# Kernel tuning notes

Measured on AMD Instinct MI355X. Metric: run time of the kernel, lower is better.

Reference implementation:

```python
import jax, jax.numpy as jnp
import numpy as np

IN_FEATURES = 4096
OUT_FEATURES = 16384


def setup_inputs() -> dict:
    key = jax.random.key(0)
    k_x, k_w = jax.random.split(key)
    x = jax.random.normal(k_x, (8192, IN_FEATURES), dtype=jnp.float32)
    weight = jax.random.normal(k_w, (OUT_FEATURES, IN_FEATURES), dtype=jnp.float32)
    return {"x": x, "weight": weight}


def ternary_quantize(weight):
    # scale = mean(|W|) clamped; quantize to {-1,0,1}*scale
    scale = jnp.maximum(jnp.mean(jnp.abs(weight)), 1e-8)
    q = jnp.round(jnp.clip(weight / scale, -1.0, 1.0)) * scale
    return q


def reference(x, weight):
    qw = ternary_quantize(weight)  # [out, in]
    # F.linear: x @ W^T
    return jnp.einsum('ti,oi->to', x, qw)
```

## Files before the change

### kernel.cpp

```cpp
#include <hip/hip_runtime.h>
#include <hip/hip_bf16.h>
#include <stdint.h>

typedef __attribute__((ext_vector_type(4))) int i32x4;

#define M_DIM 8192
#define K_DIM 4096
#define N_DIM 16384
#define NELEM_W ((long)N_DIM * (long)K_DIM)
#define NELEM_X ((long)M_DIM * (long)K_DIM)


__device__ __forceinline__ void g2l16(const void* g, void* l) {
  __builtin_amdgcn_global_load_lds(
      (const __attribute__((address_space(1))) unsigned int*)g,
      (__attribute__((address_space(3))) unsigned int*)l, 16, 0, 0);
}


__global__ void reduce_absw(const float4* __restrict__ w4, double* __restrict__ partials, int n4) {
  const int tid = threadIdx.x;
  double s = 0.0;
  const int stride = gridDim.x * blockDim.x;
  for (int i = blockIdx.x * blockDim.x + tid; i < n4; i += stride) {
    float4 v = w4[i];
    s += (double)fabsf(v.x);
    s += (double)fabsf(v.y);
    s += (double)fabsf(v.z);
    s += (double)fabsf(v.w);
  }
  __shared__ double sd[256];
  sd[tid] = s;
  __syncthreads();
  for (int off = 128; off > 0; off >>= 1) {
    if (tid < off) sd[tid] += sd[tid + off];
    __syncthreads();
  }
  if (tid == 0) partials[blockIdx.x] = sd[0];
}

__global__ void finalize_scale(const double* __restrict__ partials, float* __restrict__ sp) {
  const int tid = threadIdx.x;
  double s = 0.0;
#pragma unroll
  for (int j = 0; j < 8; ++j) s += partials[tid * 8 + j];
  __shared__ double sd[256];
  sd[tid] = s;
  __syncthreads();
  for (int off = 128; off > 0; off >>= 1) {
    if (tid < off) sd[tid] += sd[tid + off];
    __syncthreads();
  }
  if (tid == 0) {
    double mean = sd[0] / (double)NELEM_W;
    float sc = (float)mean;
    if (sc < 1e-8f) sc = 1e-8f;
    sp[0] = sc;
  }
}


__global__ void quant_w_i8(const float4* __restrict__ w4, char* __restrict__ q,
                           const float* __restrict__ sp, int n4) {
  const float sc = sp[0];
  const int stride = gridDim.x * blockDim.x;
  for (int i = blockIdx.x * blockDim.x + threadIdx.x; i < n4; i += stride) {
    float4 v = w4[i];
    char4 o;
    o.x = (char)rintf(fminf(fmaxf(v.x / sc, -1.f), 1.f));
    o.y = (char)rintf(fminf(fmaxf(v.y / sc, -1.f), 1.f));
    o.z = (char)rintf(fminf(fmaxf(v.z / sc, -1.f), 1.f));
    o.w = (char)rintf(fminf(fmaxf(v.w / sc, -1.f), 1.f));
    *(char4*)(q + (long)i * 4) = o;
  }
}


__global__ __launch_bounds__(256)
void quant_x_i8(const float* __restrict__ x, char* __restrict__ xq,
                float* __restrict__ s_row) {
  const int row = blockIdx.x;
  const int tid = threadIdx.x;
  const float4* xr = (const float4*)(x + (long)row * K_DIM);
  float4 v[4];
  float m = 0.f;
#pragma unroll
  for (int k = 0; k < 4; ++k) {
    v[k] = xr[tid + 256 * k];
    m = fmaxf(m, fmaxf(fmaxf(fabsf(v[k].x), fabsf(v[k].y)),
                       fmaxf(fabsf(v[k].z), fabsf(v[k].w))));
  }
  __shared__ float red[256];
  red[tid] = m;
  __syncthreads();
  for (int off = 128; off > 0; off >>= 1) {
    if (tid < off) red[tid] = fmaxf(red[tid], red[tid + off]);
    __syncthreads();
  }
  const float mx = red[0];
  const float inv = (mx > 0.f) ? (127.f / mx) : 0.f;
  if (tid == 0) s_row[row] = (mx > 0.f) ? (mx / 127.f) : 0.f;
  char4* out = (char4*)(xq + (long)row * K_DIM);
#pragma unroll
  for (int k = 0; k < 4; ++k) {
    char4 o;
    o.x = (char)fminf(fmaxf(rintf(v[k].x * inv), -127.f), 127.f);
    o.y = (char)fminf(fmaxf(rintf(v[k].y * inv), -127.f), 127.f);
    o.z = (char)fminf(fmaxf(rintf(v[k].z * inv), -127.f), 127.f);
    o.w = (char)fminf(fmaxf(rintf(v[k].w * inv), -127.f), 127.f);
    out[tid + 256 * k] = o;
  }
}


template<int MH, int NH>
__device__ __forceinline__ void mfmaq(i32x4 (&acc)[8][4], const i32x4 (&a)[8], const i32x4 (&bfr)[8]) {
#pragma unroll
  for (int im = 0; im < 4; ++im) {
#pragma unroll
    for (int in = 0; in < 2; ++in) {
      const int m = MH * 4 + im, n = NH * 2 + in;
      acc[m][n] = __builtin_amdgcn_mfma_i32_16x16x64_i8(a[im * 2 + 0], bfr[n * 2 + 0], acc[m][n], 0, 0, 0);
      acc[m][n] = __builtin_amdgcn_mfma_i32_16x16x64_i8(a[im * 2 + 1], bfr[n * 2 + 1], acc[m][n], 0, 0, 0);
    }
  }
}

#define FENCE asm volatile("" ::: "memory")
#define BAR do { FENCE; __builtin_amdgcn_s_barrier(); FENCE; } while (0)
#define VMW6 asm volatile("s_waitcnt vmcnt(6)" ::: "memory")
#define VMW0 asm volatile("s_waitcnt vmcnt(0)" ::: "memory")
#define PRIO1 __builtin_amdgcn_s_setprio(1)
#define PRIO0 __builtin_amdgcn_s_setprio(0)

#define STG_A(bb, h, kt) do { \
    const char* g_ = Ac + aG + (unsigned)(h) * 524288u + (unsigned)(kt) * 128u; \
    char* l_ = lds + (unsigned)(bb) * 32768u + (unsigned)(h) * 16384u + ldsT; \
    g2l16(g_, l_); g2l16(g_ + 262144u, l_ + 8192u); \
  } while (0)
#define STG_B(bb, h, kt) do { \
    const char* g_ = Bc + bG + (unsigned)(h) * 524288u + (unsigned)(kt) * 128u; \
    char* l_ = lds + 65536u + (unsigned)(bb) * 32768u + (unsigned)(h) * 16384u + ldsT; \
    g2l16(g_, l_); g2l16(g_ + 262144u, l_ + 8192u); \
  } while (0)

#define LDA_(d, bb, m, ks) d = *(const i32x4*)(lds + Abase##bb + (unsigned)(m) * 2048u + frk + coff##ks)
#define LDB_(d, bb, n, ks) d = *(const i32x4*)(lds + Bbase##bb + (unsigned)(n) * 2048u + frk + coff##ks)

#define RD_A03(bb) do { \
    LDA_(a[0], bb, 0, 0); LDA_(a[1], bb, 0, 1); LDA_(a[2], bb, 1, 0); LDA_(a[3], bb, 1, 1); \
    LDA_(a[4], bb, 2, 0); LDA_(a[5], bb, 2, 1); LDA_(a[6], bb, 3, 0); LDA_(a[7], bb, 3, 1); \
  } while (0)
#define RD_A47(bb) do { \
    LDA_(a[0], bb, 4, 0); LDA_(a[1], bb, 4, 1); LDA_(a[2], bb, 5, 0); LDA_(a[3], bb, 5, 1); \
    LDA_(a[4], bb, 6, 0); LDA_(a[5], bb, 6, 1); LDA_(a[6], bb, 7, 0); LDA_(a[7], bb, 7, 1); \
  } while (0)
#define RD_BALL(bb) do { \
    LDB_(bfr[0], bb, 0, 0); LDB_(bfr[1], bb, 0, 1); LDB_(bfr[2], bb, 1, 0); LDB_(bfr[3], bb, 1, 1); \
    LDB_(bfr[4], bb, 2, 0); LDB_(bfr[5], bb, 2, 1); LDB_(bfr[6], bb, 3, 0); LDB_(bfr[7], bb, 3, 1); \
  } while (0)

#define MFMA_PHASE(MH, NH) do { BAR; PRIO1; mfmaq<MH, NH>(acc, a, bfr); PRIO0; BAR; } while (0)

__global__ __launch_bounds__(512, 2)
void gemm_i8(const char* __restrict__ A, const char* __restrict__ B,
             float* __restrict__ C, const float* __restrict__ sp,
             const float* __restrict__ s_row) {
  extern __shared__ char lds[];

  const int tid = threadIdx.x;
  const int wave = tid >> 6, lane = tid & 63;
  const int fr = lane & 15, fq = lane >> 4;
  const int wr = wave >> 2;
  const int wc = wave & 3;

  int wgid = blockIdx.x;
  wgid = (wgid & 7) * ((int)gridDim.x >> 3) + (wgid >> 3);
  const int bm = wgid >> 6;
  const int bn = wgid & 63;

  const int r0 = tid >> 3;
  const int pslot = tid & 7;
  const int lslot = pslot ^ (r0 & 7);
  const unsigned aG = (unsigned)(bm * 256 + r0) * (unsigned)K_DIM + (unsigned)lslot * 16u;
  const unsigned bG = (unsigned)(bn * 256 + r0) * (unsigned)K_DIM + (unsigned)lslot * 16u;
  const unsigned ldsT = (unsigned)tid * 16u;
  const char* Ac = A;
  const char* Bc = B;

  const unsigned axor = (unsigned)(fr & 7) << 4;
  const unsigned coff0 = ((unsigned)(fq * 16)) ^ axor;
  const unsigned coff1 = ((unsigned)(64 + fq * 16)) ^ axor;
  const unsigned frk = (unsigned)fr * 128u;
  const unsigned Abase0 = (unsigned)(wr * 16384);
  const unsigned Abase1 = (unsigned)(32768 + wr * 16384);
  const unsigned Bhalf = (unsigned)(65536 + (wc >> 1) * 16384 + (wc & 1) * 8192);
  const unsigned Bbase0 = Bhalf;
  const unsigned Bbase1 = Bhalf + 32768u;

  i32x4 acc[8][4] = {};
  i32x4 a[8], bfr[8];

  STG_A(0, 0, 0); STG_A(0, 1, 0);
  STG_B(0, 0, 0); STG_B(0, 1, 0);
  STG_B(1, 0, 1); STG_B(1, 1, 1); STG_A(1, 0, 1);
  VMW6;
  BAR;

#pragma unroll 1
  for (int i = 0; i < 15; ++i) {
    const int t1 = 2 * i + 1, t2 = 2 * i + 2, t3 = 2 * i + 3;

    RD_A03(0); RD_BALL(0);
    STG_A(1, 1, t1);
    MFMA_PHASE(0, 0);
    STG_B(0, 0, t2);
    MFMA_PHASE(0, 1);
    RD_A47(0);
    STG_B(0, 1, t2);
    MFMA_PHASE(1, 1);
    STG_A(0, 0, t2);
    VMW6;
    MFMA_PHASE(1, 0);
    RD_A03(1); RD_BALL(1);
    STG_A(0, 1, t2);
    MFMA_PHASE(0, 0);
    STG_B(1, 0, t3);
    MFMA_PHASE(0, 1);
    RD_A47(1);
    STG_B(1, 1, t3);
    MFMA_PHASE(1, 1);
    STG_A(1, 0, t3);
    VMW6;
    MFMA_PHASE(1, 0);
  }

  {
    RD_A03(0); RD_BALL(0);
    STG_A(1, 1, 31);
    MFMA_PHASE(0, 0);
    MFMA_PHASE(0, 1);
    RD_A47(0);
    MFMA_PHASE(1, 1);
    VMW0;
    MFMA_PHASE(1, 0);
    RD_A03(1); RD_BALL(1);
    MFMA_PHASE(0, 0);
    MFMA_PHASE(0, 1);
    RD_A47(1);
    MFMA_PHASE(1, 1);
    MFMA_PHASE(1, 0);
  }

  const float sw = sp[0];
  const int crow0 = bm * 256 + wr * 128 + fq * 4;
  const int ccol0 = bn * 256 + wc * 64 + fr;
#pragma unroll
  for (int m = 0; m < 8; ++m) {
#pragma unroll
    for (int j = 0; j < 4; ++j) {
      const int row = crow0 + m * 16 + j;
      const float sc = s_row[row] * sw;
#pragma unroll
      for (int n = 0; n < 4; ++n) {
        C[(long)row * N_DIM + (ccol0 + n * 16)] = (float)acc[m][n][j] * sc;
      }
    }
  }
}


typedef __hip_bfloat16 bf16;
typedef __attribute__((ext_vector_type(8))) short short8;
typedef __attribute__((ext_vector_type(4))) float f32x4;

__device__ __forceinline__ unsigned short f2bf(float f) {
  unsigned int u = __float_as_uint(f);
  u += 0x7FFFu + ((u >> 16) & 1u);
  return (unsigned short)(u >> 16);
}

__global__ __launch_bounds__(256)
void gemm_fly(const float* __restrict__ X, const float* __restrict__ W,
              float* __restrict__ C, const float* __restrict__ sp) {
  __shared__ alignas(16) bf16 As[128 * 32];
  __shared__ alignas(16) bf16 Bs[128 * 32];

  const int tid = threadIdx.x;
  const int wave = tid >> 6;
  const int lane = tid & 63;

  int wgid = blockIdx.x;
  wgid = (wgid & 7) * ((int)gridDim.x >> 3) + (wgid >> 3);
  const int nbn = N_DIM / 128;
  const int bm = wgid / nbn;
  const int bn = wgid % nbn;

  const float sc = sp[0];

  const int wr = (wave >> 1) * 64;
  const int wc = (wave & 1) * 64;
  const int fr = lane & 15;
  const int fq = lane >> 4;
  const char* AsB = (const char*)As;
  const char* BsB = (const char*)Bs;
  const unsigned aoff = (unsigned)((wr + fr) * 64 + fq * 16);
  const unsigned boff = (unsigned)((wc + fr) * 64 + fq * 16);

  f32x4 acc[4][4] = {};

  for (int kt = 0; kt < K_DIM; kt += 32) {
#pragma unroll
    for (int r = 0; r < 4; ++r) {
      int e = r * 1024 + tid * 4;
      int row = e >> 5;
      int k4 = e & 31;
      float4 xv = *(const float4*)(X + (long)(bm * 128 + row) * K_DIM + kt + k4);
      ushort4 xb;
      xb.x = f2bf(xv.x); xb.y = f2bf(xv.y); xb.z = f2bf(xv.z); xb.w = f2bf(xv.w);
      *(ushort4*)(As + e) = xb;
      float4 wv = *(const float4*)(W + (long)(bn * 128 + row) * K_DIM + kt + k4);
      ushort4 wb;
      wb.x = f2bf(rintf(fminf(fmaxf(wv.x / sc, -1.f), 1.f)));
      wb.y = f2bf(rintf(fminf(fmaxf(wv.y / sc, -1.f), 1.f)));
      wb.z = f2bf(rintf(fminf(fmaxf(wv.z / sc, -1.f), 1.f)));
      wb.w = f2bf(rintf(fminf(fmaxf(wv.w / sc, -1.f), 1.f)));
      *(ushort4*)(Bs + e) = wb;
    }
    __syncthreads();

    short8 a[4], b[4];
#pragma unroll
    for (int m = 0; m < 4; ++m)
      a[m] = *(const short8*)(AsB + aoff + m * (16 * 64));
#pragma unroll
    for (int n = 0; n < 4; ++n)
      b[n] = *(const short8*)(BsB + boff + n * (16 * 64));
#pragma unroll
    for (int m = 0; m < 4; ++m)
#pragma unroll
      for (int n = 0; n < 4; ++n)
        acc[m][n] = __builtin_amdgcn_mfma_f32_16x16x32_bf16(a[m], b[n], acc[m][n], 0, 0, 0);

    __syncthreads();
  }

  const long crow0 = (long)(bm * 128 + wr + fq * 4);
  const int ccol0 = bn * 128 + wc + fr;
#pragma unroll
  for (int m = 0; m < 4; ++m)
#pragma unroll
    for (int n = 0; n < 4; ++n)
#pragma unroll
      for (int j = 0; j < 4; ++j) {
        long row = crow0 + (long)(m * 16 + j);
        int col = ccol0 + n * 16;
        C[row * N_DIM + col] = acc[m][n][j] * sc;
      }
}


extern "C" void kernel_launch(void* const* d_in, const int* in_sizes, int n_in,
                              void* d_out, int out_size, void* d_ws, size_t ws_size,
                              hipStream_t stream) {
  const float* x = (const float*)d_in[0];
  const float* w = (const float*)d_in[1];
  float* out = (float*)d_out;

  char* ws = (char*)d_ws;
  double* partials = (double*)ws;
  float* sp = (float*)(ws + 16384);
  const size_t SROW_OFF = 32768;
  const size_t WQ_OFF = SROW_OFF + 32768;
  const size_t XQ_OFF = WQ_OFF + (size_t)NELEM_W;
  const size_t NEEDED = XQ_OFF + (size_t)NELEM_X;

  reduce_absw<<<2048, 256, 0, stream>>>((const float4*)w, partials, (int)(NELEM_W / 4));
  finalize_scale<<<1, 256, 0, stream>>>(partials, sp);

  if (ws_size >= NEEDED) {
    float* s_row = (float*)(ws + SROW_OFF);
    char* wq = ws + WQ_OFF;
    char* xq = ws + XQ_OFF;
    quant_w_i8<<<2048, 256, 0, stream>>>((const float4*)w, wq, sp, (int)(NELEM_W / 4));
    quant_x_i8<<<M_DIM, 256, 0, stream>>>(x, xq, s_row);

    static const int lds_bytes = 131072;
    (void)hipFuncSetAttribute((const void*)gemm_i8,
                              hipFuncAttributeMaxDynamicSharedMemorySize, lds_bytes);
    const int grid = (M_DIM / 256) * (N_DIM / 256);
    gemm_i8<<<grid, 512, lds_bytes, stream>>>(xq, wq, out, sp, s_row);
  } else {
    const int grid = (M_DIM / 128) * (N_DIM / 128);
    gemm_fly<<<grid, 256, 0, stream>>>(x, w, out, sp);
  }
}
```

Baseline: 681.1 us.

## Switch int8 GEMM to 32x32x32 MFMA with reworked LDS reads and barriers

Replaces the 16x16x64 int8 MFMA tiles with 32x32x32 int8 MFMA, cutting the number of MFMA instructions and LDS fragment loads per wave. Fragment reads are regrouped into two phases per buffer with explicit lgkmcnt waits, and each MFMA group now has a single barrier instead of two. The epilogue is rewritten for the 32x32 accumulator layout. Fewer barriers and reads should reduce stalls, but this risks LDS bank conflicts with the new lane mapping and ordering hazards from the looser synchronisation.

```diff
diff --git a/kernel.cpp b/kernel.cpp
--- a/kernel.cpp
+++ b/kernel.cpp
@@ -3,6 +3,7 @@
 #include <stdint.h>
 
 typedef __attribute__((ext_vector_type(4))) int i32x4;
+typedef __attribute__((ext_vector_type(16))) int i32x16;
 
 #define M_DIM 8192
 #define K_DIM 4096
@@ -113,23 +114,11 @@
 }
 
 
-template<int MH, int NH>
-__device__ __forceinline__ void mfmaq(i32x4 (&acc)[8][4], const i32x4 (&a)[8], const i32x4 (&bfr)[8]) {
-#pragma unroll
-  for (int im = 0; im < 4; ++im) {
-#pragma unroll
-    for (int in = 0; in < 2; ++in) {
-      const int m = MH * 4 + im, n = NH * 2 + in;
-      acc[m][n] = __builtin_amdgcn_mfma_i32_16x16x64_i8(a[im * 2 + 0], bfr[n * 2 + 0], acc[m][n], 0, 0, 0);
-      acc[m][n] = __builtin_amdgcn_mfma_i32_16x16x64_i8(a[im * 2 + 1], bfr[n * 2 + 1], acc[m][n], 0, 0, 0);
-    }
-  }
-}
-
 #define FENCE asm volatile("" ::: "memory")
 #define BAR do { FENCE; __builtin_amdgcn_s_barrier(); FENCE; } while (0)
 #define VMW6 asm volatile("s_waitcnt vmcnt(6)" ::: "memory")
 #define VMW0 asm volatile("s_waitcnt vmcnt(0)" ::: "memory")
+#define LGKM0 asm volatile("s_waitcnt lgkmcnt(0)" ::: "memory")
 #define PRIO1 __builtin_amdgcn_s_setprio(1)
 #define PRIO0 __builtin_amdgcn_s_setprio(0)
 
@@ -144,23 +133,33 @@
     g2l16(g_, l_); g2l16(g_ + 262144u, l_ + 8192u); \
   } while (0)
 
-#define LDA_(d, bb, m, ks) d = *(const i32x4*)(lds + Abase##bb + (unsigned)(m) * 2048u + frk + coff##ks)
-#define LDB_(d, bb, n, ks) d = *(const i32x4*)(lds + Bbase##bb + (unsigned)(n) * 2048u + frk + coff##ks)
-
-#define RD_A03(bb) do { \
-    LDA_(a[0], bb, 0, 0); LDA_(a[1], bb, 0, 1); LDA_(a[2], bb, 1, 0); LDA_(a[3], bb, 1, 1); \
-    LDA_(a[4], bb, 2, 0); LDA_(a[5], bb, 2, 1); LDA_(a[6], bb, 3, 0); LDA_(a[7], bb, 3, 1); \
-  } while (0)
-#define RD_A47(bb) do { \
-    LDA_(a[0], bb, 4, 0); LDA_(a[1], bb, 4, 1); LDA_(a[2], bb, 5, 0); LDA_(a[3], bb, 5, 1); \
-    LDA_(a[4], bb, 6, 0); LDA_(a[5], bb, 6, 1); LDA_(a[6], bb, 7, 0); LDA_(a[7], bb, 7, 1); \
-  } while (0)
-#define RD_BALL(bb) do { \
-    LDB_(bfr[0], bb, 0, 0); LDB_(bfr[1], bb, 0, 1); LDB_(bfr[2], bb, 1, 0); LDB_(bfr[3], bb, 1, 1); \
-    LDB_(bfr[4], bb, 2, 0); LDB_(bfr[5], bb, 2, 1); LDB_(bfr[6], bb, 3, 0); LDB_(bfr[7], bb, 3, 1); \
-  } while (0)
-
-#define MFMA_PHASE(MH, NH) do { BAR; PRIO1; mfmaq<MH, NH>(acc, a, bfr); PRIO0; BAR; } while (0)
+#define RD_P1(Ar, Br) do { \
+    b[0] = *(const i32x4*)(lds + (Br) + cof0);          a[0] = *(const i32x4*)(lds + (Ar) + cof0); \
+    a[4] = *(const i32x4*)(lds + (Ar) + 4096u + cof0); \
+    b[1] = *(const i32x4*)(lds + (Br) + cof1);          a[1] = *(const i32x4*)(lds + (Ar) + cof1); \
+    a[5] = *(const i32x4*)(lds + (Ar) + 4096u + cof1); \
+    b[2] = *(const i32x4*)(lds + (Br) + cof2);          a[2] = *(const i32x4*)(lds + (Ar) + cof2); \
+    a[6] = *(const i32x4*)(lds + (Ar) + 4096u + cof2); \
+    b[3] = *(const i32x4*)(lds + (Br) + cof3);          a[3] = *(const i32x4*)(lds + (Ar) + cof3); \
+    a[7] = *(const i32x4*)(lds + (Ar) + 4096u + cof3); \
+    b[4] = *(const i32x4*)(lds + (Br) + 4096u + cof0);  b[5] = *(const i32x4*)(lds + (Br) + 4096u + cof1); \
+    b[6] = *(const i32x4*)(lds + (Br) + 4096u + cof2);  b[7] = *(const i32x4*)(lds + (Br) + 4096u + cof3); \
+  } while (0)
+
+#define RD_P3(Ar) do { \
+    a[0] = *(const i32x4*)(lds + (Ar) + 8192u + cof0);  a[4] = *(const i32x4*)(lds + (Ar) + 12288u + cof0); \
+    a[1] = *(const i32x4*)(lds + (Ar) + 8192u + cof1);  a[5] = *(const i32x4*)(lds + (Ar) + 12288u + cof1); \
+    a[2] = *(const i32x4*)(lds + (Ar) + 8192u + cof2);  a[6] = *(const i32x4*)(lds + (Ar) + 12288u + cof2); \
+    a[3] = *(const i32x4*)(lds + (Ar) + 8192u + cof3);  a[7] = *(const i32x4*)(lds + (Ar) + 12288u + cof3); \
+  } while (0)
+
+#define MF8(NH, accA, accB) do { \
+    _Pragma("unroll") \
+    for (int ks = 0; ks < 4; ++ks) { \
+      accA = __builtin_amdgcn_mfma_i32_32x32x32_i8(a[ks],     b[(NH) * 4 + ks], accA, 0, 0, 0); \
+      accB = __builtin_amdgcn_mfma_i32_32x32x32_i8(a[4 + ks], b[(NH) * 4 + ks], accB, 0, 0, 0); \
+    } \
+  } while (0)
 
 __global__ __launch_bounds__(512, 2)
 void gemm_i8(const char* __restrict__ A, const char* __restrict__ B,
@@ -170,7 +169,8 @@
 
   const int tid = threadIdx.x;
   const int wave = tid >> 6, lane = tid & 63;
-  const int fr = lane & 15, fq = lane >> 4;
+  const int rl = lane & 31;
+  const int kh = lane >> 5;
   const int wr = wave >> 2;
   const int wc = wave & 3;
 
@@ -188,18 +188,21 @@
   const char* Ac = A;
   const char* Bc = B;
 
-  const unsigned axor = (unsigned)(fr & 7) << 4;
-  const unsigned coff0 = ((unsigned)(fq * 16)) ^ axor;
-  const unsigned coff1 = ((unsigned)(64 + fq * 16)) ^ axor;
-  const unsigned frk = (unsigned)fr * 128u;
-  const unsigned Abase0 = (unsigned)(wr * 16384);
-  const unsigned Abase1 = (unsigned)(32768 + wr * 16384);
-  const unsigned Bhalf = (unsigned)(65536 + (wc >> 1) * 16384 + (wc & 1) * 8192);
-  const unsigned Bbase0 = Bhalf;
-  const unsigned Bbase1 = Bhalf + 32768u;
-
-  i32x4 acc[8][4] = {};
-  i32x4 a[8], bfr[8];
+  const unsigned x7 = (unsigned)(lane & 7);
+  const unsigned cof0 = ((0u | (unsigned)kh) ^ x7) << 4;
+  const unsigned cof1 = ((2u | (unsigned)kh) ^ x7) << 4;
+  const unsigned cof2 = ((4u | (unsigned)kh) ^ x7) << 4;
+  const unsigned cof3 = ((6u | (unsigned)kh) ^ x7) << 4;
+  const unsigned frk = (unsigned)rl * 128u;
+  const unsigned A0r = (unsigned)(wr * 16384) + frk;
+  const unsigned A1r = 32768u + (unsigned)(wr * 16384) + frk;
+  const unsigned bofs = (unsigned)((wc >> 1) * 16384 + (wc & 1) * 8192);
+  const unsigned B0r = 65536u + bofs + frk;
+  const unsigned B1r = 98304u + bofs + frk;
+
+  i32x16 c00 = {}, c01 = {}, c10 = {}, c11 = {};
+  i32x16 c20 = {}, c21 = {}, c30 = {}, c31 = {};
+  i32x4 a[8], b[8];
 
   STG_A(0, 0, 0); STG_A(0, 1, 0);
   STG_B(0, 0, 0); STG_B(0, 1, 0);
@@ -211,62 +214,80 @@
   for (int i = 0; i < 15; ++i) {
     const int t1 = 2 * i + 1, t2 = 2 * i + 2, t3 = 2 * i + 3;
 
-    RD_A03(0); RD_BALL(0);
     STG_A(1, 1, t1);
-    MFMA_PHASE(0, 0);
+    RD_P1(A0r, B0r);
+    PRIO1; MF8(0, c00, c10); PRIO0;
+    LGKM0;
+    BAR;
     STG_B(0, 0, t2);
-    MFMA_PHASE(0, 1);
-    RD_A47(0);
+    PRIO1; MF8(1, c01, c11); PRIO0;
+    BAR;
     STG_B(0, 1, t2);
-    MFMA_PHASE(1, 1);
+    RD_P3(A0r);
+    PRIO1; MF8(1, c21, c31); PRIO0;
+    BAR;
     STG_A(0, 0, t2);
+    PRIO1; MF8(0, c20, c30); PRIO0;
     VMW6;
-    MFMA_PHASE(1, 0);
-    RD_A03(1); RD_BALL(1);
+    BAR;
     STG_A(0, 1, t2);
-    MFMA_PHASE(0, 0);
+    RD_P1(A1r, B1r);
+    PRIO1; MF8(0, c00, c10); PRIO0;
+    LGKM0;
+    BAR;
     STG_B(1, 0, t3);
-    MFMA_PHASE(0, 1);
-    RD_A47(1);
+    PRIO1; MF8(1, c01, c11); PRIO0;
+    BAR;
     STG_B(1, 1, t3);
-    MFMA_PHASE(1, 1);
+    RD_P3(A1r);
+    PRIO1; MF8(1, c21, c31); PRIO0;
+    BAR;
     STG_A(1, 0, t3);
+    PRIO1; MF8(0, c20, c30); PRIO0;
     VMW6;
-    MFMA_PHASE(1, 0);
+    BAR;
   }
 
   {
-    RD_A03(0); RD_BALL(0);
     STG_A(1, 1, 31);
-    MFMA_PHASE(0, 0);
-    MFMA_PHASE(0, 1);
-    RD_A47(0);
-    MFMA_PHASE(1, 1);
+    RD_P1(A0r, B0r);
+    PRIO1; MF8(0, c00, c10); PRIO0;
+    LGKM0;
+    BAR;
+    PRIO1; MF8(1, c01, c11); PRIO0;
+    BAR;
+    RD_P3(A0r);
+    PRIO1; MF8(1, c21, c31); PRIO0;
+    BAR;
+    PRIO1; MF8(0, c20, c30); PRIO0;
     VMW0;
-    MFMA_PHASE(1, 0);
-    RD_A03(1); RD_BALL(1);
-    MFMA_PHASE(0, 0);
-    MFMA_PHASE(0, 1);
-    RD_A47(1);
-    MFMA_PHASE(1, 1);
-    MFMA_PHASE(1, 0);
+    BAR;
+    RD_P1(A1r, B1r);
+    PRIO1; MF8(0, c00, c10); PRIO0;
+    PRIO1; MF8(1, c01, c11); PRIO0;
+    RD_P3(A1r);
+    PRIO1; MF8(1, c21, c31); PRIO0;
+    PRIO1; MF8(0, c20, c30); PRIO0;
   }
 
   const float sw = sp[0];
-  const int crow0 = bm * 256 + wr * 128 + fq * 4;
-  const int ccol0 = bn * 256 + wc * 64 + fr;
-#pragma unroll
-  for (int m = 0; m < 8; ++m) {
-#pragma unroll
-    for (int j = 0; j < 4; ++j) {
-      const int row = crow0 + m * 16 + j;
-      const float sc = s_row[row] * sw;
-#pragma unroll
-      for (int n = 0; n < 4; ++n) {
-        C[(long)row * N_DIM + (ccol0 + n * 16)] = (float)acc[m][n][j] * sc;
-      }
-    }
-  }
+  const int crow0 = bm * 256 + wr * 128;
+  const int ccol0 = bn * 256 + wc * 64;
+#define EPI2(ccA, ccB, mt) do { \
+    _Pragma("unroll") \
+    for (int r = 0; r < 16; ++r) { \
+      const int grow = crow0 + (mt) * 32 + (r & 3) + 8 * (r >> 2) + 4 * kh; \
+      const float scl = s_row[grow] * sw; \
+      float* rowp = C + (long)grow * N_DIM + ccol0 + rl; \
+      rowp[0]  = (float)ccA[r] * scl; \
+      rowp[32] = (float)ccB[r] * scl; \
+    } \
+  } while (0)
+  EPI2(c00, c01, 0);
+  EPI2(c10, c11, 1);
+  EPI2(c20, c21, 2);
+  EPI2(c30, c31, 3);
+#undef EPI2
 }
 
 
```

Measured after the change: 1.785 ms. 2.62x slower.

## Halve barriers per MFMA phase and interleave LDS reads with MFMA issue

Applied to the files above, without the earlier changes.

Replaces the two-barriers-per-phase MFMA_PHASE macro with a schedule of one barrier per phase. Global-to-LDS stages and LDS fragment reads now issue before or between MFMA groups, with explicit lgkmcnt(0) waits only where a buffer is about to be overwritten. The aim is to cut barrier stalls and let LDS traffic overlap the matrix-core work. The risk is a race if the reordered barriers no longer protect the double-buffered LDS tiles, and the compiler may still insert its own waits.

```diff
diff --git a/kernel.cpp b/kernel.cpp
--- a/kernel.cpp
+++ b/kernel.cpp
@@ -130,6 +130,7 @@
 #define BAR do { FENCE; __builtin_amdgcn_s_barrier(); FENCE; } while (0)
 #define VMW6 asm volatile("s_waitcnt vmcnt(6)" ::: "memory")
 #define VMW0 asm volatile("s_waitcnt vmcnt(0)" ::: "memory")
+#define LGKM0 asm volatile("s_waitcnt lgkmcnt(0)" ::: "memory")
 #define PRIO1 __builtin_amdgcn_s_setprio(1)
 #define PRIO0 __builtin_amdgcn_s_setprio(0)
 
@@ -160,8 +161,6 @@
     LDB_(bfr[4], bb, 2, 0); LDB_(bfr[5], bb, 2, 1); LDB_(bfr[6], bb, 3, 0); LDB_(bfr[7], bb, 3, 1); \
   } while (0)
 
-#define MFMA_PHASE(MH, NH) do { BAR; PRIO1; mfmaq<MH, NH>(acc, a, bfr); PRIO0; BAR; } while (0)
-
 __global__ __launch_bounds__(512, 2)
 void gemm_i8(const char* __restrict__ A, const char* __restrict__ B,
              float* __restrict__ C, const float* __restrict__ sp,
@@ -211,45 +210,60 @@
   for (int i = 0; i < 15; ++i) {
     const int t1 = 2 * i + 1, t2 = 2 * i + 2, t3 = 2 * i + 3;
 
+    STG_A(1, 1, t1);
     RD_A03(0); RD_BALL(0);
-    STG_A(1, 1, t1);
-    MFMA_PHASE(0, 0);
+    PRIO1; mfmaq<0, 0>(acc, a, bfr); PRIO0;
+    LGKM0;
+    BAR;
     STG_B(0, 0, t2);
-    MFMA_PHASE(0, 1);
+    PRIO1; mfmaq<0, 1>(acc, a, bfr); PRIO0;
+    BAR;
+    STG_B(0, 1, t2);
     RD_A47(0);
-    STG_B(0, 1, t2);
-    MFMA_PHASE(1, 1);
+    PRIO1; mfmaq<1, 1>(acc, a, bfr); PRIO0;
+    BAR;
     STG_A(0, 0, t2);
+    PRIO1; mfmaq<1, 0>(acc, a, bfr); PRIO0;
     VMW6;
-    MFMA_PHASE(1, 0);
+    BAR;
+    STG_A(0, 1, t2);
     RD_A03(1); RD_BALL(1);
-    STG_A(0, 1, t2);
-    MFMA_PHASE(0, 0);
+    PRIO1; mfmaq<0, 0>(acc, a, bfr); PRIO0;
+    LGKM0;
+    BAR;
     STG_B(1, 0, t3);
-    MFMA_PHASE(0, 1);
+    PRIO1; mfmaq<0, 1>(acc, a, bfr); PRIO0;
+    BAR;
+    STG_B(1, 1, t3);
     RD_A47(1);
-    STG_B(1, 1, t3);
-    MFMA_PHASE(1, 1);
+    PRIO1; mfmaq<1, 1>(acc, a, bfr); PRIO0;
+    BAR;
     STG_A(1, 0, t3);
+    PRIO1; mfmaq<1, 0>(acc, a, bfr); PRIO0;
     VMW6;
-    MFMA_PHASE(1, 0);
+    BAR;
   }
 
   {
+    STG_A(1, 1, 31);
     RD_A03(0); RD_BALL(0);
-    STG_A(1, 1, 31);
-    MFMA_PHASE(0, 0);
-    MFMA_PHASE(0, 1);
+    PRIO1; mfmaq<0, 0>(acc, a, bfr); PRIO0;
+    LGKM0;
+    BAR;
+    PRIO1; mfmaq<0, 1>(acc, a, bfr); PRIO0;
+    BAR;
     RD_A47(0);
-    MFMA_PHASE(1, 1);
+    PRIO1; mfmaq<1, 1>(acc, a, bfr); PRIO0;
+    BAR;
+    PRIO1; mfmaq<1, 0>(acc, a, bfr); PRIO0;
     VMW0;
-    MFMA_PHASE(1, 0);
+    BAR;
     RD_A03(1); RD_BALL(1);
-    MFMA_PHASE(0, 0);
-    MFMA_PHASE(0, 1);
+    PRIO1; mfmaq<0, 0>(acc, a, bfr); PRIO0;
+    PRIO1; mfmaq<0, 1>(acc, a, bfr); PRIO0;
     RD_A47(1);
-    MFMA_PHASE(1, 1);
-    MFMA_PHASE(1, 0);
+    PRIO1; mfmaq<1, 1>(acc, a, bfr); PRIO0;
+    PRIO1; mfmaq<1, 0>(acc, a, bfr); PRIO0;
   }
 
   const float sw = sp[0];
```

Result: no change. 668.2 us (median of 2 runs) (-1.9%).

## Replace barrier-phased ping-pong schedule with per-tile double buffering and 2x2 MFMA blocks

Applied to the files above, without the earlier changes.

Drops the eight-phase schedule, which put two barriers around every MFMA group and interleaved the global-to-LDS stages. Each K tile now issues all next-tile loads up front, then runs fine-grained 2x2 MFMA blocks interleaved with smaller LDS fragment reads, and uses one full vmcnt(0) wait plus one barrier per tile. This removes many barriers and lets LDS reads overlap MFMA work. The cost is losing the partial vmcnt overlap of global loads and waiting for every load to finish before each tile switch.

```diff
diff --git a/kernel.cpp b/kernel.cpp
--- a/kernel.cpp
+++ b/kernel.cpp
@@ -113,22 +113,20 @@
 }
 
 
-template<int MH, int NH>
-__device__ __forceinline__ void mfmaq(i32x4 (&acc)[8][4], const i32x4 (&a)[8], const i32x4 (&bfr)[8]) {
-#pragma unroll
-  for (int im = 0; im < 4; ++im) {
-#pragma unroll
-    for (int in = 0; in < 2; ++in) {
-      const int m = MH * 4 + im, n = NH * 2 + in;
-      acc[m][n] = __builtin_amdgcn_mfma_i32_16x16x64_i8(a[im * 2 + 0], bfr[n * 2 + 0], acc[m][n], 0, 0, 0);
-      acc[m][n] = __builtin_amdgcn_mfma_i32_16x16x64_i8(a[im * 2 + 1], bfr[n * 2 + 1], acc[m][n], 0, 0, 0);
-    }
-  }
+template<int MP, int NP, int AH>
+__device__ __forceinline__ void mb(i32x4 (&acc)[8][4], const i32x4 (&a)[8], const i32x4 (&b)[8]) {
+#pragma unroll
+  for (int dm = 0; dm < 2; ++dm)
+#pragma unroll
+    for (int dn = 0; dn < 2; ++dn)
+#pragma unroll
+      for (int ks = 0; ks < 2; ++ks)
+        acc[MP * 2 + dm][NP * 2 + dn] = __builtin_amdgcn_mfma_i32_16x16x64_i8(
+            a[AH + dm * 2 + ks], b[NP * 4 + dn * 2 + ks], acc[MP * 2 + dm][NP * 2 + dn], 0, 0, 0);
 }
 
 #define FENCE asm volatile("" ::: "memory")
 #define BAR do { FENCE; __builtin_amdgcn_s_barrier(); FENCE; } while (0)
-#define VMW6 asm volatile("s_waitcnt vmcnt(6)" ::: "memory")
 #define VMW0 asm volatile("s_waitcnt vmcnt(0)" ::: "memory")
 #define PRIO1 __builtin_amdgcn_s_setprio(1)
 #define PRIO0 __builtin_amdgcn_s_setprio(0)
@@ -147,20 +145,30 @@
 #define LDA_(d, bb, m, ks) d = *(const i32x4*)(lds + Abase##bb + (unsigned)(m) * 2048u + frk + coff##ks)
 #define LDB_(d, bb, n, ks) d = *(const i32x4*)(lds + Bbase##bb + (unsigned)(n) * 2048u + frk + coff##ks)
 
-#define RD_A03(bb) do { \
-    LDA_(a[0], bb, 0, 0); LDA_(a[1], bb, 0, 1); LDA_(a[2], bb, 1, 0); LDA_(a[3], bb, 1, 1); \
-    LDA_(a[4], bb, 2, 0); LDA_(a[5], bb, 2, 1); LDA_(a[6], bb, 3, 0); LDA_(a[7], bb, 3, 1); \
-  } while (0)
-#define RD_A47(bb) do { \
-    LDA_(a[0], bb, 4, 0); LDA_(a[1], bb, 4, 1); LDA_(a[2], bb, 5, 0); LDA_(a[3], bb, 5, 1); \
-    LDA_(a[4], bb, 6, 0); LDA_(a[5], bb, 6, 1); LDA_(a[6], bb, 7, 0); LDA_(a[7], bb, 7, 1); \
-  } while (0)
-#define RD_BALL(bb) do { \
-    LDB_(bfr[0], bb, 0, 0); LDB_(bfr[1], bb, 0, 1); LDB_(bfr[2], bb, 1, 0); LDB_(bfr[3], bb, 1, 1); \
-    LDB_(bfr[4], bb, 2, 0); LDB_(bfr[5], bb, 2, 1); LDB_(bfr[6], bb, 3, 0); LDB_(bfr[7], bb, 3, 1); \
-  } while (0)
-
-#define MFMA_PHASE(MH, NH) do { BAR; PRIO1; mfmaq<MH, NH>(acc, a, bfr); PRIO0; BAR; } while (0)
+#define RD_A(AH, bb, mp) do { \
+    LDA_(a[(AH) + 0], bb, 2 * (mp) + 0, 0); LDA_(a[(AH) + 1], bb, 2 * (mp) + 0, 1); \
+    LDA_(a[(AH) + 2], bb, 2 * (mp) + 1, 0); LDA_(a[(AH) + 3], bb, 2 * (mp) + 1, 1); \
+  } while (0)
+#define RD_B(bb, np) do { \
+    LDB_(b[4 * (np) + 0], bb, 2 * (np) + 0, 0); LDB_(b[4 * (np) + 1], bb, 2 * (np) + 0, 1); \
+    LDB_(b[4 * (np) + 2], bb, 2 * (np) + 1, 0); LDB_(b[4 * (np) + 3], bb, 2 * (np) + 1, 1); \
+  } while (0)
+
+#define TILE(bb, obb, kt1, DO_STG) do { \
+    if (DO_STG) { STG_A(obb, 0, kt1); STG_A(obb, 1, kt1); STG_B(obb, 0, kt1); STG_B(obb, 1, kt1); } \
+    RD_A(0, bb, 0); RD_B(bb, 0); \
+    PRIO1; mb<0, 0, 0>(acc, a, b); PRIO0; \
+    RD_A(4, bb, 1); RD_B(bb, 1); \
+    PRIO1; mb<0, 1, 0>(acc, a, b); PRIO0; \
+    RD_A(0, bb, 2); \
+    PRIO1; mb<1, 1, 4>(acc, a, b); PRIO0; \
+    PRIO1; mb<1, 0, 4>(acc, a, b); PRIO0; \
+    RD_A(4, bb, 3); \
+    PRIO1; mb<2, 0, 0>(acc, a, b); PRIO0; \
+    PRIO1; mb<2, 1, 0>(acc, a, b); PRIO0; \
+    PRIO1; mb<3, 1, 4>(acc, a, b); PRIO0; \
+    PRIO1; mb<3, 0, 4>(acc, a, b); PRIO0; \
+  } while (0)
 
 __global__ __launch_bounds__(512, 2)
 void gemm_i8(const char* __restrict__ A, const char* __restrict__ B,
@@ -199,58 +207,22 @@
   const unsigned Bbase1 = Bhalf + 32768u;
 
   i32x4 acc[8][4] = {};
-  i32x4 a[8], bfr[8];
-
-  STG_A(0, 0, 0); STG_A(0, 1, 0);
-  STG_B(0, 0, 0); STG_B(0, 1, 0);
-  STG_B(1, 0, 1); STG_B(1, 1, 1); STG_A(1, 0, 1);
-  VMW6;
+  i32x4 a[8], b[8];
+
+  STG_A(0, 0, 0); STG_A(0, 1, 0); STG_B(0, 0, 0); STG_B(0, 1, 0);
+  VMW0;
   BAR;
 
 #pragma unroll 1
   for (int i = 0; i < 15; ++i) {
-    const int t1 = 2 * i + 1, t2 = 2 * i + 2, t3 = 2 * i + 3;
-
-    RD_A03(0); RD_BALL(0);
-    STG_A(1, 1, t1);
-    MFMA_PHASE(0, 0);
-    STG_B(0, 0, t2);
-    MFMA_PHASE(0, 1);
-    RD_A47(0);
-    STG_B(0, 1, t2);
-    MFMA_PHASE(1, 1);
-    STG_A(0, 0, t2);
-    VMW6;
-    MFMA_PHASE(1, 0);
-    RD_A03(1); RD_BALL(1);
-    STG_A(0, 1, t2);
-    MFMA_PHASE(0, 0);
-    STG_B(1, 0, t3);
-    MFMA_PHASE(0, 1);
-    RD_A47(1);
-    STG_B(1, 1, t3);
-    MFMA_PHASE(1, 1);
-    STG_A(1, 0, t3);
-    VMW6;
-    MFMA_PHASE(1, 0);
-  }
-
-  {
-    RD_A03(0); RD_BALL(0);
-    STG_A(1, 1, 31);
-    MFMA_PHASE(0, 0);
-    MFMA_PHASE(0, 1);
-    RD_A47(0);
-    MFMA_PHASE(1, 1);
-    VMW0;
-    MFMA_PHASE(1, 0);
-    RD_A03(1); RD_BALL(1);
-    MFMA_PHASE(0, 0);
-    MFMA_PHASE(0, 1);
-    RD_A47(1);
-    MFMA_PHASE(1, 1);
-    MFMA_PHASE(1, 0);
-  }
+    TILE(0, 1, 2 * i + 1, true);
+    VMW0; BAR;
+    TILE(1, 0, 2 * i + 2, true);
+    VMW0; BAR;
+  }
+  TILE(0, 1, 31, true);
+  VMW0; BAR;
+  TILE(1, 0, 0, false);
 
   const float sw = sp[0];
   const int crow0 = bm * 256 + wr * 128 + fq * 4;
```

Result: slower. 696.7 us (+2.3%).
